# Optimization experiments

Measured on AMD Instinct MI355X. Metric: run time of the kernel, lower is better.

The kernel has to match this reference:

```python
import jax, jax.numpy as jnp
import numpy as np

NC, NG, D = 50000, 3000, 64
E_CG, E_GC, E_GG = 3_000_000, 3_000_000, 100_000
KEEP = 0.9  # 1 - drop_out


def _mask(key, n):
    return (jax.random.uniform(key, (n, 1)) < KEEP).astype(jnp.float32) / KEEP


def setup_inputs() -> dict:
    key = jax.random.key(0)
    ks = jax.random.split(key, 20)
    return {
        "c_feat": jax.random.normal(ks[0], (NC, D), jnp.float32),
        "g_feat": jax.random.normal(ks[1], (NG, D), jnp.float32),
        "cj_cell": jax.random.uniform(ks[2], (NC, 1), jnp.float32),
        "ci_cell": jax.random.uniform(ks[3], (NC, 1), jnp.float32),
        "cj_gene": jax.random.uniform(ks[4], (NG, 1), jnp.float32),
        "ci_gene": jax.random.uniform(ks[5], (NG, 1), jnp.float32),
        "cjj_gene": jax.random.uniform(ks[6], (NG, 1), jnp.float32),
        "cii_gene": jax.random.uniform(ks[7], (NG, 1), jnp.float32),
        "mask_exp": _mask(ks[8], NC),
        "mask_rev": _mask(ks[9], NG),
        "mask_gg": _mask(ks[10], NG),
        "src_cg": jax.random.randint(ks[11], (E_CG,), 0, NC, jnp.int32),
        "dst_cg": jax.random.randint(ks[12], (E_CG,), 0, NG, jnp.int32),
        "src_gc": jax.random.randint(ks[13], (E_GC,), 0, NG, jnp.int32),
        "dst_gc": jax.random.randint(ks[14], (E_GC,), 0, NC, jnp.int32),
        "src_gg": jax.random.randint(ks[15], (E_GG,), 0, NG, jnp.int32),
        "dst_gg": jax.random.randint(ks[16], (E_GG,), 0, NG, jnp.int32),
    }


def _light_conv(src_feats, cj, mask, ci, src, dst, n_dst):
    # weighted_feats = src_feats * dropout(cj); copy_u + sum; scale by ci
    wf = src_feats * (cj * mask)                      # [Nsrc, D]
    agg = jax.ops.segment_sum(wf[src], dst, num_segments=n_dst)  # [Ndst, D]
    return agg * ci


def reference(c_feat, g_feat, cj_cell, ci_cell, cj_gene, ci_gene,
              cjj_gene, cii_gene, mask_exp, mask_rev, mask_gg,
              src_cg, dst_cg, src_gc, dst_gc, src_gg, dst_gg):
    alpha1 = 0.5
    # relation 'exp': cell -> gene
    g_exp = _light_conv(c_feat, cj_cell, mask_exp, ci_gene, src_cg, dst_cg, NG)
    # relation 'reverse-exp': gene -> cell (only relation targeting cells)
    c_out = _light_conv(g_feat, cj_gene, mask_rev, ci_cell, src_gc, dst_gc, NC)
    # relation 'co-exp': gene -> gene (uses cjj/cii)
    g_gg = _light_conv(g_feat, cjj_gene, mask_gg, cii_gene, src_gg, dst_gg, NG)
    # aggregate='stack' over gene dst relations, then alpha-weighted combine
    g_out = alpha1 * g_exp + (1.0 - alpha1) * g_gg
    return (c_out, g_out)
```

## Files before the change

kernel.cpp:

```cpp
#include <hip/hip_runtime.h>

#define NC 50000
#define NG 3000
#define D  64

#define NB_CG 750
#define NB_GC 782
#define PBITS 18
#define TILE  4096
#define KTILE (TILE / 256)
#define NPREP 128
#define CAP   4608
#define KCAP  ((CAP + 255) / 256)
#define GG_CAP 128
#define OVF_CAP 262144

__device__ inline unsigned short f2bf(float x) {
    unsigned u = __float_as_uint(x);
    unsigned r = u + 0x7FFFu + ((u >> 16) & 1u);
    return (unsigned short)(r >> 16);
}

__device__ __forceinline__ void acc8(const uint4& q, float f[8]) {
    f[0] += __uint_as_float(q.x << 16); f[1] += __uint_as_float(q.x & 0xFFFF0000u);
    f[2] += __uint_as_float(q.y << 16); f[3] += __uint_as_float(q.y & 0xFFFF0000u);
    f[4] += __uint_as_float(q.z << 16); f[5] += __uint_as_float(q.z & 0xFFFF0000u);
    f[6] += __uint_as_float(q.w << 16); f[7] += __uint_as_float(q.w & 0xFFFF0000u);
}

__device__ inline void row8f(const float* feat, int s, int l8, float f[8]) {
    const float4* row = (const float4*)(feat + (size_t)s * D);
    const float4 a = row[l8];
    const float4 b = row[l8 + 8];
    f[0] = a.x; f[1] = a.y; f[2] = a.z; f[3] = a.w;
    f[4] = b.x; f[5] = b.y; f[6] = b.z; f[7] = b.w;
}


__global__ __launch_bounds__(256, 7) void partition_kernel(
    const int* __restrict__ src_cg, const int* __restrict__ dst_cg, int e_cg, int nt_cg,
    const int* __restrict__ src_gc, const int* __restrict__ dst_gc, int e_gc, int nt_gc,
    const int* __restrict__ src_gg, const int* __restrict__ dst_gg, int e_gg,
    int* __restrict__ cur_cg, int* __restrict__ cur_gc, int* __restrict__ cnt_gg,
    unsigned* __restrict__ bkt_cg, unsigned* __restrict__ bkt_gc, int* __restrict__ bkt_gg,
    int* __restrict__ ovf_cnt, uint2* __restrict__ ovf,
    const float* __restrict__ cj_cell, const float* __restrict__ mask_exp,
    const float* __restrict__ cj_gene, const float* __restrict__ mask_rev,
    const float* __restrict__ cjj_gene, const float* __restrict__ mask_gg,
    float* __restrict__ w_cell, float* __restrict__ w_rev, float* __restrict__ w_gg,
    const float* __restrict__ c_feat, const float* __restrict__ g_feat,
    unsigned short* __restrict__ wc16, unsigned short* __restrict__ wg16,
    unsigned short* __restrict__ wgg16, int do_cvt)
{
    const int tid = threadIdx.x;
    const int NT2 = nt_cg + nt_gc;

    if (blockIdx.x >= NT2 + 64) {
        const int pb = blockIdx.x - NT2 - 64;
        const long long stride = (long long)NPREP * 256;
        for (long long i = (long long)pb * 256 + tid; i < NC; i += stride)
            w_cell[i] = cj_cell[i] * mask_exp[i];
        for (long long i = (long long)pb * 256 + tid; i < NG; i += stride) {
            w_rev[i] = cj_gene[i] * mask_rev[i];
            w_gg[i]  = cjj_gene[i] * mask_gg[i];
        }
        if (do_cvt) {
            const long long total8 = (long long)(NC + NG) * D / 8;
            for (long long t = (long long)pb * 256 + tid; t < total8; t += stride) {
                const long long base = t * 8;
                if (base < (long long)NC * D) {
                    const int s = (int)(base >> 6);
                    const float w = cj_cell[s] * mask_exp[s];
                    const float4 a = ((const float4*)(c_feat + base))[0];
                    const float4 b = ((const float4*)(c_feat + base))[1];
                    unsigned short* dp = wc16 + base;
                    ((ushort4*)dp)[0] = make_ushort4(f2bf(w*a.x), f2bf(w*a.y), f2bf(w*a.z), f2bf(w*a.w));
                    ((ushort4*)dp)[1] = make_ushort4(f2bf(w*b.x), f2bf(w*b.y), f2bf(w*b.z), f2bf(w*b.w));
                } else {
                    const long long gb = base - (long long)NC * D;
                    const int s = (int)(gb >> 6);
                    const float wr = cj_gene[s] * mask_rev[s];
                    const float wg = cjj_gene[s] * mask_gg[s];
                    const float4 a = ((const float4*)(g_feat + gb))[0];
                    const float4 b = ((const float4*)(g_feat + gb))[1];
                    ((ushort4*)(wg16 + gb))[0]  = make_ushort4(f2bf(wr*a.x), f2bf(wr*a.y), f2bf(wr*a.z), f2bf(wr*a.w));
                    ((ushort4*)(wg16 + gb))[1]  = make_ushort4(f2bf(wr*b.x), f2bf(wr*b.y), f2bf(wr*b.z), f2bf(wr*b.w));
                    ((ushort4*)(wgg16 + gb))[0] = make_ushort4(f2bf(wg*a.x), f2bf(wg*a.y), f2bf(wg*a.z), f2bf(wg*a.w));
                    ((ushort4*)(wgg16 + gb))[1] = make_ushort4(f2bf(wg*b.x), f2bf(wg*b.y), f2bf(wg*b.z), f2bf(wg*b.w));
                }
            }
            if (pb == 0) {
                for (int i = tid; i < D; i += 256) {
                    wc16[(size_t)NC * D + i] = 0;
                    wg16[(size_t)NG * D + i] = 0;
                    wgg16[(size_t)NG * D + i] = 0;
                }
            }
        }
        return;
    }

    if (blockIdx.x >= NT2) {
        for (long long e = (long long)(blockIdx.x - NT2) * 256 + tid; e < e_gg;
             e += (long long)64 * 256) {
            const int dd = dst_gg[e];
            const int ss = src_gg[e];
            if ((unsigned)dd >= (unsigned)NG || (unsigned)ss >= (unsigned)NG) continue;
            const int pos = atomicAdd(&cnt_gg[dd], 1);
            if (pos < GG_CAP) bkt_gg[dd * GG_CAP + pos] = ss;
            else {
                const int op = atomicAdd(ovf_cnt, 1);
                if (op >= 0 && op < OVF_CAP)
                    ovf[op] = make_uint2((2u << 30) | (unsigned)ss, (unsigned)dd);
            }
        }
        return;
    }

    const int* src; const int* dst; int ne; int* cur; unsigned* bkt;
    int shift, nbins, t; unsigned rel;
    if (blockIdx.x < nt_cg) { src = src_cg; dst = dst_cg; ne = e_cg; cur = cur_cg; bkt = bkt_cg; shift = 2; nbins = NB_CG; t = blockIdx.x;         rel = 0u; }
    else                    { src = src_gc; dst = dst_gc; ne = e_gc; cur = cur_gc; bkt = bkt_gc; shift = 6; nbins = NB_GC; t = blockIdx.x - nt_cg; rel = 1u; }
    const long long tb = (long long)t * TILE;
    if (tb >= ne) return;
    const int n = (int)((ne - tb) < TILE ? (ne - tb) : TILE);

    __shared__ int toff[784];
    __shared__ int gsadj[784];
    __shared__ unsigned staged[TILE];
    const unsigned PMASK = (1u << PBITS) - 1u;
    const unsigned DMASK = (1u << shift) - 1u;

    for (int i = tid; i < nbins; i += 256) toff[i] = 0;

    int rd[KTILE], rs[KTILE];
    #pragma unroll
    for (int k = 0; k < KTILE; ++k) {
        const int i = k * 256 + tid;
        rd[k] = (i < n) ? dst[tb + i] : -1;
        rs[k] = (i < n) ? src[tb + i] : 0;
    }
    __syncthreads();
    #pragma unroll
    for (int k = 0; k < KTILE; ++k) {
        const unsigned b = ((unsigned)rd[k]) >> shift;
        if (b < (unsigned)nbins) atomicAdd(&toff[b], 1);
    }
    __syncthreads();
    if (tid < 64) {
        int carry = 0;
        for (int c = 0; c < nbins; c += 64) {
            int idx = c + tid;
            int v = (idx < nbins) ? toff[idx] : 0;
            int incl = v;
            #pragma unroll
            for (int d = 1; d < 64; d <<= 1) {
                int x = __shfl_up(incl, d);
                if (tid >= d) incl += x;
            }
            if (idx < nbins) {
                const int excl = incl - v + carry;
                toff[idx] = excl;
                gsadj[idx] = (v ? atomicAdd(&cur[idx], v) : 0) - excl;
            }
            carry += __shfl(incl, 63);
        }
    }
    __syncthreads();
    #pragma unroll
    for (int k = 0; k < KTILE; ++k) {
        const unsigned d = (unsigned)rd[k];
        const unsigned b = d >> shift;
        if (b < (unsigned)nbins) {
            const int p = atomicAdd(&toff[b], 1);
            if (p >= 0 && p < TILE)
                staged[p] = (b << PBITS) | ((unsigned)rs[k] << shift) | (d & DMASK);
        }
    }
    __syncthreads();
    for (int i = tid; i < n; i += 256) {
        const unsigned v = staged[i];
        const unsigned b = v >> PBITS;
        if (b < (unsigned)nbins) {
            const int local = gsadj[b] + i;
            if (local >= 0 && local < CAP) {
                bkt[(size_t)b * CAP + local] = v & PMASK;
            } else {
                const unsigned s = (v >> shift) & 0xFFFFu;
                const unsigned dd = (b << shift) | (v & DMASK);
                const int op = atomicAdd(ovf_cnt, 1);
                if (op >= 0 && op < OVF_CAP)
                    ovf[op] = make_uint2((rel << 30) | s, dd);
            }
        }
    }
}


template <bool BF16>
__global__ __launch_bounds__(256, 8) void gather3_kernel(
    const unsigned* __restrict__ bkt_cg, const int* __restrict__ cur_cg,
    const unsigned* __restrict__ bkt_gc, const int* __restrict__ cur_gc,
    const void* __restrict__ fc, const void* __restrict__ fg, const void* __restrict__ fgg,
    const float* __restrict__ craw, const float* __restrict__ graw,
    const float* __restrict__ w_cell, const float* __restrict__ w_rev, const float* __restrict__ w_gg,
    const float* __restrict__ ci_gene, const float* __restrict__ cii_gene, const float* __restrict__ ci_cell,
    const int* __restrict__ cnt_gg, const int* __restrict__ bkt_gg,
    const int* __restrict__ ovf_cnt, const uint2* __restrict__ ovf,
    float* __restrict__ g_out, float* __restrict__ c_out)
{
    __shared__ unsigned short sorted[CAP];
    __shared__ int lh[64];
    __shared__ int loff[64];

    const bool is_cg = (blockIdx.x < NB_CG);
    const int bin = is_cg ? blockIdx.x : blockIdx.x - NB_CG;
    int n = (is_cg ? cur_cg : cur_gc)[bin];
    n = n > CAP ? CAP : n;
    const long long base = (long long)bin * CAP;
    const unsigned* bkt = is_cg ? bkt_cg : bkt_gc;
    const void* feat = is_cg ? fc : fg;
    const float* wsrc = is_cg ? w_cell : w_rev;
    const int shift = is_cg ? 2 : 6;
    const int DIVv = is_cg ? 4 : 64;
    const int KPC  = is_cg ? 16 : 1;
    const int DUM  = is_cg ? NC : NG;
    const int tid  = threadIdx.x;
    const int lane = tid & 63;
    const int wid  = tid >> 6;
    const int grp8 = lane >> 3;
    const int l8   = lane & 7;

    for (int i = tid; i < 64; i += 256) lh[i] = 0;
    unsigned rv[KCAP];
    #pragma unroll
    for (int k = 0; k < KCAP; ++k) {
        const int i = k * 256 + tid;
        rv[k] = (i < n) ? bkt[base + i] : 0xFFFFFFFFu;
    }
    __syncthreads();
    #pragma unroll
    for (int k = 0; k < KCAP; ++k) {
        const unsigned v = rv[k];
        if (v != 0xFFFFFFFFu) {
            const int kk = is_cg ? (int)(((v & 3u) << 4) | (((v >> 2) & 0xFFFFu) >> 12))
                                 : (int)(v & 63u);
            atomicAdd(&lh[kk], 1);
        }
    }
    __syncthreads();
    if (tid < 64) {
        int v = lh[tid];
        int incl = v;
        #pragma unroll
        for (int d = 1; d < 64; d <<= 1) {
            int t = __shfl_up(incl, d);
            if (tid >= d) incl += t;
        }
        loff[tid] = incl - v;
        lh[tid] = 0;
    }
    __syncthreads();
    #pragma unroll
    for (int k = 0; k < KCAP; ++k) {
        const unsigned v = rv[k];
        if (v != 0xFFFFFFFFu) {
            const int kk = is_cg ? (int)(((v & 3u) << 4) | (((v >> 2) & 0xFFFFu) >> 12))
                                 : (int)(v & 63u);
            const int p = loff[kk] + atomicAdd(&lh[kk], 1);
            if (p >= 0 && p < CAP) sorted[p] = (unsigned short)((v >> shift) & 0xFFFFu);
        }
    }
    __syncthreads();

    int novf = *ovf_cnt;
    novf = novf < 0 ? 0 : (novf > OVF_CAP ? OVF_CAP : novf);

    for (int cell = wid; cell < DIVv; cell += 4) {
        const int r = (bin << shift) + cell;
        if (r >= (is_cg ? NG : NC)) continue;

        float fA[8] = {0.f, 0.f, 0.f, 0.f, 0.f, 0.f, 0.f, 0.f};
        {
            const int k0 = cell * KPC, k1 = k0 + KPC - 1;
            const int lo = loff[k0], hi = loff[k1] + lh[k1];
            if (BF16) {
                const uint4* fp = (const uint4*)feat;
                for (int jj = lo; jj < hi; jj += 32) {
                    const int b0 = jj + grp8;
                    const int s0 = (b0      < hi) ? (int)sorted[b0]      : DUM;
                    const int s1 = (b0 + 8  < hi) ? (int)sorted[b0 + 8]  : DUM;
                    const int s2 = (b0 + 16 < hi) ? (int)sorted[b0 + 16] : DUM;
                    const int s3 = (b0 + 24 < hi) ? (int)sorted[b0 + 24] : DUM;
                    const uint4 q0 = fp[(size_t)s0 * 8 + l8];
                    const uint4 q1 = fp[(size_t)s1 * 8 + l8];
                    const uint4 q2 = fp[(size_t)s2 * 8 + l8];
                    const uint4 q3 = fp[(size_t)s3 * 8 + l8];
                    acc8(q0, fA); acc8(q1, fA); acc8(q2, fA); acc8(q3, fA);
                }
            } else {
                for (int jj = lo; jj < hi; jj += 8) {
                    const int j = jj + grp8;
                    const bool valid = (j < hi);
                    const int s = valid ? (int)sorted[j] : 0;
                    const float w = valid ? wsrc[s] : 0.0f;
                    float f[8]; row8f((const float*)feat, s, l8, f);
                    #pragma unroll
                    for (int q = 0; q < 8; ++q) fA[q] += w * f[q];
                }
            }
        }

        float fB[8] = {0.f, 0.f, 0.f, 0.f, 0.f, 0.f, 0.f, 0.f};
        if (is_cg) {
            int ngg = cnt_gg[r];
            ngg = ngg > GG_CAP ? GG_CAP : ngg;
            const int* bg = bkt_gg + (size_t)r * GG_CAP;
            if (BF16) {
                const uint4* fp = (const uint4*)fgg;
                for (int jj = 0; jj < ngg; jj += 16) {
                    const int j0 = jj + grp8;
                    const int j1 = jj + 8 + grp8;
                    const int s0 = (j0 < ngg) ? bg[j0] : NG;
                    const int s1 = (j1 < ngg) ? bg[j1] : NG;
                    const uint4 q0 = fp[(size_t)s0 * 8 + l8];
                    const uint4 q1 = fp[(size_t)s1 * 8 + l8];
                    acc8(q0, fB); acc8(q1, fB);
                }
            } else {
                for (int jj = 0; jj < ngg; jj += 8) {
                    const int j = jj + grp8;
                    const bool valid = (j < ngg);
                    const int s = valid ? bg[j] : 0;
                    const float w = valid ? w_gg[s] : 0.0f;
                    float f[8]; row8f(graw, s, l8, f);
                    #pragma unroll
                    for (int q = 0; q < 8; ++q) fB[q] += w * f[q];
                }
            }
        }

        #pragma unroll
        for (int q = 0; q < 8; ++q) {
            #pragma unroll
            for (int off = 8; off < 64; off <<= 1) fA[q] += __shfl_xor(fA[q], off);
        }
        if (is_cg) {
            #pragma unroll
            for (int q = 0; q < 8; ++q) {
                #pragma unroll
                for (int off = 8; off < 64; off <<= 1) fB[q] += __shfl_xor(fB[q], off);
            }
        }

        if (grp8 == 0) {
            float o[8];
            float* outp;
            if (is_cg) {
                const float sa = 0.5f * ci_gene[r];
                const float sb = 0.5f * cii_gene[r];
                outp = g_out + (size_t)r * D;
                #pragma unroll
                for (int q = 0; q < 8; ++q) o[q] = sa * fA[q] + sb * fB[q];
            } else {
                const float sc = ci_cell[r];
                outp = c_out + (size_t)r * D;
                #pragma unroll
                for (int q = 0; q < 8; ++q) o[q] = sc * fA[q];
            }

            if (novf > 0) {
                for (int e = 0; e < novf; ++e) {
                    const uint2 vv = ovf[e];
                    const int d = (int)vv.y;
                    if (d != r) continue;
                    const unsigned relv = vv.x >> 30;
                    const int s = (int)(vv.x & 0x3FFFFFFFu);
                    const float* fr = nullptr; float w = 0.f;
                    if (is_cg) {
                        if (relv == 0u && s < NC)      { fr = craw + (size_t)s * D; w = 0.5f * ci_gene[r] * w_cell[s]; }
                        else if (relv == 2u && s < NG) { fr = graw + (size_t)s * D; w = 0.5f * cii_gene[r] * w_gg[s]; }
                    } else {
                        if (relv == 1u && s < NG)      { fr = graw + (size_t)s * D; w = ci_cell[r] * w_rev[s]; }
                    }
                    if (fr) {
                        #pragma unroll
                        for (int q = 0; q < 8; ++q) {
                            const int elem = BF16 ? (8 * l8 + q)
                                                  : (q < 4 ? 4 * l8 + q : 32 + 4 * l8 + (q - 4));
                            o[q] += w * fr[elem];
                        }
                    }
                }
            }

            if (BF16) {
                *(float4*)(outp + 8 * l8)     = make_float4(o[0], o[1], o[2], o[3]);
                *(float4*)(outp + 8 * l8 + 4) = make_float4(o[4], o[5], o[6], o[7]);
            } else {
                *(float4*)(outp + 4 * l8)      = make_float4(o[0], o[1], o[2], o[3]);
                *(float4*)(outp + 32 + 4 * l8) = make_float4(o[4], o[5], o[6], o[7]);
            }
        }
    }
}


__global__ __launch_bounds__(256) void edge_scatter_kernel(
    const float* __restrict__ feat, const float* __restrict__ cj,
    const float* __restrict__ mask, const float* __restrict__ ci,
    const int* __restrict__ src, const int* __restrict__ dst,
    float* __restrict__ out, int nedges, float alpha)
{
    const int lane16 = threadIdx.x & 15;
    const int eloc   = threadIdx.x >> 4;
    const long long e = (long long)blockIdx.x * 16 + eloc;
    if (e >= nedges) return;
    const int s = src[e];
    const int t = dst[e];
    const float w = cj[s] * mask[s] * ci[t] * alpha;
    const float4 v = *(const float4*)(feat + (size_t)s * D + lane16 * 4);
    float* o = out + (size_t)t * D + lane16 * 4;
#if defined(__HIP_DEVICE_COMPILE__)
    unsafeAtomicAdd(o + 0, w * v.x);
    unsafeAtomicAdd(o + 1, w * v.y);
    unsafeAtomicAdd(o + 2, w * v.z);
    unsafeAtomicAdd(o + 3, w * v.w);
#endif
}


extern "C" void kernel_launch(void* const* d_in, const int* in_sizes, int n_in,
                              void* d_out, int out_size, void* d_ws, size_t ws_size,
                              hipStream_t stream)
{
    const float* c_feat   = (const float*)d_in[0];
    const float* g_feat   = (const float*)d_in[1];
    const float* cj_cell  = (const float*)d_in[2];
    const float* ci_cell  = (const float*)d_in[3];
    const float* cj_gene  = (const float*)d_in[4];
    const float* ci_gene  = (const float*)d_in[5];
    const float* cjj_gene = (const float*)d_in[6];
    const float* cii_gene = (const float*)d_in[7];
    const float* mask_exp = (const float*)d_in[8];
    const float* mask_rev = (const float*)d_in[9];
    const float* mask_gg  = (const float*)d_in[10];
    const int*   src_cg   = (const int*)d_in[11];
    const int*   dst_cg   = (const int*)d_in[12];
    const int*   src_gc   = (const int*)d_in[13];
    const int*   dst_gc   = (const int*)d_in[14];
    const int*   src_gg   = (const int*)d_in[15];
    const int*   dst_gg   = (const int*)d_in[16];

    const int e_cg = in_sizes[11];
    const int e_gc = in_sizes[13];
    const int e_gg = in_sizes[15];

    float* c_out = (float*)d_out;
    float* g_out = (float*)d_out + (size_t)NC * D;

    const int nt_cg = (e_cg + TILE - 1) / TILE;
    const int nt_gc = (e_gc + TILE - 1) / TILE;

    int* ws = (int*)d_ws;
    size_t p = 0;
    int* cur_cg  = ws + p; p += NB_CG;
    int* cur_gc  = ws + p; p += NB_GC;
    int* cnt_gg  = ws + p; p += NG;
    int* ovf_cnt = ws + p; p += 1;
    const size_t zcount = p;
    float* w_cell = (float*)(ws + p); p += NC;
    float* w_rev  = (float*)(ws + p); p += NG;
    float* w_gg   = (float*)(ws + p); p += NG;
    unsigned* bkt_cg = (unsigned*)(ws + p); p += (size_t)NB_CG * CAP;
    unsigned* bkt_gc = (unsigned*)(ws + p); p += (size_t)NB_GC * CAP;
    int* bkt_gg = ws + p; p += (size_t)NG * GG_CAP;
    p = (p + 1) & ~(size_t)1;
    uint2* ovf = (uint2*)(ws + p); p += (size_t)OVF_CAP * 2;
    const size_t need_base = p * sizeof(int);
    p = (p + 3) & ~(size_t)3;
    unsigned short* wc16  = (unsigned short*)(ws + p); p += (size_t)(NC + 1) * D / 2;
    unsigned short* wg16  = (unsigned short*)(ws + p); p += (size_t)(NG + 1) * D / 2;
    unsigned short* wgg16 = (unsigned short*)(ws + p); p += (size_t)(NG + 1) * D / 2;
    const size_t need_full = p * sizeof(int);

    if (need_base > ws_size || e_cg > 3200000 || e_gc > 3200000 || e_gg > 200000) {
        hipMemsetAsync(d_out, 0, (size_t)out_size * sizeof(float), stream);
        edge_scatter_kernel<<<(e_cg + 15) / 16, 256, 0, stream>>>(
            c_feat, cj_cell, mask_exp, ci_gene, src_cg, dst_cg, g_out, e_cg, 0.5f);
        edge_scatter_kernel<<<(e_gc + 15) / 16, 256, 0, stream>>>(
            g_feat, cj_gene, mask_rev, ci_cell, src_gc, dst_gc, c_out, e_gc, 1.0f);
        edge_scatter_kernel<<<(e_gg + 15) / 16, 256, 0, stream>>>(
            g_feat, cjj_gene, mask_gg, cii_gene, src_gg, dst_gg, g_out, e_gg, 0.5f);
        return;
    }
    const int use_bf16 = (need_full <= ws_size) ? 1 : 0;

    hipMemsetAsync(ws, 0, zcount * sizeof(int), stream);

    partition_kernel<<<nt_cg + nt_gc + 64 + NPREP, 256, 0, stream>>>(
        src_cg, dst_cg, e_cg, nt_cg,
        src_gc, dst_gc, e_gc, nt_gc,
        src_gg, dst_gg, e_gg,
        cur_cg, cur_gc, cnt_gg,
        bkt_cg, bkt_gc, bkt_gg,
        ovf_cnt, ovf,
        cj_cell, mask_exp, cj_gene, mask_rev, cjj_gene, mask_gg,
        w_cell, w_rev, w_gg, c_feat, g_feat, wc16, wg16, wgg16, use_bf16);

    if (use_bf16) {
        gather3_kernel<true><<<NB_CG + NB_GC, 256, 0, stream>>>(
            bkt_cg, cur_cg, bkt_gc, cur_gc,
            (const void*)wc16, (const void*)wg16, (const void*)wgg16,
            c_feat, g_feat,
            w_cell, w_rev, w_gg, ci_gene, cii_gene, ci_cell,
            cnt_gg, bkt_gg, ovf_cnt, ovf, g_out, c_out);
    } else {
        gather3_kernel<false><<<NB_CG + NB_GC, 256, 0, stream>>>(
            bkt_cg, cur_cg, bkt_gc, cur_gc,
            (const void*)c_feat, (const void*)g_feat, (const void*)g_feat,
            c_feat, g_feat,
            w_cell, w_rev, w_gg, ci_gene, cii_gene, ci_cell,
            cnt_gg, bkt_gg, ovf_cnt, ovf, g_out, c_out);
    }
}
```

Baseline: 244.0 us.

## Split each gather bin across two blocks, using atomic accumulation for gene outputs

Launches twice as many gather blocks, each handling half of a bin. Cell-to-gene bins split their source subkeys between halves, and the two partial sums are combined into g_out with atomic adds after a memset. Gene-to-cell bins split their destination rows. This raises parallelism and occupancy for the gather phase. The cost is that each block reloads the full bucket, and it adds a g_out memset and float atomics.

```diff
diff --git a/kernel.cpp b/kernel.cpp
--- a/kernel.cpp
+++ b/kernel.cpp
@@ -213,8 +213,10 @@
     __shared__ int lh[64];
     __shared__ int loff[64];
 
-    const bool is_cg = (blockIdx.x < NB_CG);
-    const int bin = is_cg ? blockIdx.x : blockIdx.x - NB_CG;
+    const int bid = blockIdx.x;
+    const bool is_cg = (bid < 2 * NB_CG);
+    const int bin  = is_cg ? (bid >> 1) : ((bid - 2 * NB_CG) >> 1);
+    const int half = is_cg ? (bid & 1)  : ((bid - 2 * NB_CG) & 1);
     int n = (is_cg ? cur_cg : cur_gc)[bin];
     n = n > CAP ? CAP : n;
     const long long base = (long long)bin * CAP;
@@ -222,8 +224,6 @@
     const void* feat = is_cg ? fc : fg;
     const float* wsrc = is_cg ? w_cell : w_rev;
     const int shift = is_cg ? 2 : 6;
-    const int DIVv = is_cg ? 4 : 64;
-    const int KPC  = is_cg ? 16 : 1;
     const int DUM  = is_cg ? NC : NG;
     const int tid  = threadIdx.x;
     const int lane = tid & 63;
@@ -245,7 +245,8 @@
         if (v != 0xFFFFFFFFu) {
             const int kk = is_cg ? (int)(((v & 3u) << 4) | (((v >> 2) & 0xFFFFu) >> 12))
                                  : (int)(v & 63u);
-            atomicAdd(&lh[kk], 1);
+            const bool mine = is_cg ? (((kk >> 3) & 1) == half) : ((kk >> 5) == half);
+            if (mine) atomicAdd(&lh[kk], 1);
         }
     }
     __syncthreads();
@@ -267,8 +268,11 @@
         if (v != 0xFFFFFFFFu) {
             const int kk = is_cg ? (int)(((v & 3u) << 4) | (((v >> 2) & 0xFFFFu) >> 12))
                                  : (int)(v & 63u);
-            const int p = loff[kk] + atomicAdd(&lh[kk], 1);
-            if (p >= 0 && p < CAP) sorted[p] = (unsigned short)((v >> shift) & 0xFFFFu);
+            const bool mine = is_cg ? (((kk >> 3) & 1) == half) : ((kk >> 5) == half);
+            if (mine) {
+                const int p = loff[kk] + atomicAdd(&lh[kk], 1);
+                if (p >= 0 && p < CAP) sorted[p] = (unsigned short)((v >> shift) & 0xFFFFu);
+            }
         }
     }
     __syncthreads();
@@ -276,13 +280,17 @@
     int novf = *ovf_cnt;
     novf = novf < 0 ? 0 : (novf > OVF_CAP ? OVF_CAP : novf);
 
-    for (int cell = wid; cell < DIVv; cell += 4) {
+    const int cellLo = is_cg ? 0 : half * 32;
+    const int cellHi = is_cg ? 4 : half * 32 + 32;
+
+    for (int cell = cellLo + wid; cell < cellHi; cell += 4) {
         const int r = (bin << shift) + cell;
         if (r >= (is_cg ? NG : NC)) continue;
 
         float fA[8] = {0.f, 0.f, 0.f, 0.f, 0.f, 0.f, 0.f, 0.f};
         {
-            const int k0 = cell * KPC, k1 = k0 + KPC - 1;
+            const int k0 = is_cg ? (cell * 16 + 8 * half) : cell;
+            const int k1 = is_cg ? (k0 + 7) : cell;
             const int lo = loff[k0], hi = loff[k1] + lh[k1];
             if (BF16) {
                 const uint4* fp = (const uint4*)feat;
@@ -312,7 +320,7 @@
         }
 
         float fB[8] = {0.f, 0.f, 0.f, 0.f, 0.f, 0.f, 0.f, 0.f};
-        if (is_cg) {
+        if (is_cg && half == 0) {
             int ngg = cnt_gg[r];
             ngg = ngg > GG_CAP ? GG_CAP : ngg;
             const int* bg = bkt_gg + (size_t)r * GG_CAP;
@@ -345,7 +353,7 @@
             #pragma unroll
             for (int off = 8; off < 64; off <<= 1) fA[q] += __shfl_xor(fA[q], off);
         }
-        if (is_cg) {
+        if (is_cg && half == 0) {
             #pragma unroll
             for (int q = 0; q < 8; ++q) {
                 #pragma unroll
@@ -355,51 +363,71 @@
 
         if (grp8 == 0) {
             float o[8];
-            float* outp;
             if (is_cg) {
                 const float sa = 0.5f * ci_gene[r];
                 const float sb = 0.5f * cii_gene[r];
-                outp = g_out + (size_t)r * D;
                 #pragma unroll
                 for (int q = 0; q < 8; ++q) o[q] = sa * fA[q] + sb * fB[q];
+                float* outp = g_out + (size_t)r * D;
+
+                if (half == 0 && novf > 0) {
+                    for (int e = 0; e < novf; ++e) {
+                        const uint2 vv = ovf[e];
+                        if ((int)vv.y != r) continue;
+                        const unsigned relv = vv.x >> 30;
+                        const int s = (int)(vv.x & 0x3FFFFFFFu);
+                        const float* fr = nullptr; float w = 0.f;
+                        if (relv == 0u && s < NC)      { fr = craw + (size_t)s * D; w = 0.5f * ci_gene[r] * w_cell[s]; }
+                        else if (relv == 2u && s < NG) { fr = graw + (size_t)s * D; w = 0.5f * cii_gene[r] * w_gg[s]; }
+                        if (fr) {
+                            #pragma unroll
+                            for (int q = 0; q < 8; ++q) {
+                                const int elem = BF16 ? (8 * l8 + q)
+                                                      : (q < 4 ? 4 * l8 + q : 32 + 4 * l8 + (q - 4));
+                                o[q] += w * fr[elem];
+                            }
+                        }
+                    }
+                }
+#if defined(__HIP_DEVICE_COMPILE__)
+                #pragma unroll
+                for (int q = 0; q < 8; ++q) {
+                    const int elem = BF16 ? (8 * l8 + q)
+                                          : (q < 4 ? 4 * l8 + q : 32 + 4 * l8 + (q - 4));
+                    unsafeAtomicAdd(outp + elem, o[q]);
+                }
+#endif
             } else {
                 const float sc = ci_cell[r];
-                outp = c_out + (size_t)r * D;
+                float* outp = c_out + (size_t)r * D;
                 #pragma unroll
                 for (int q = 0; q < 8; ++q) o[q] = sc * fA[q];
-            }
-
-            if (novf > 0) {
-                for (int e = 0; e < novf; ++e) {
-                    const uint2 vv = ovf[e];
-                    const int d = (int)vv.y;
-                    if (d != r) continue;
-                    const unsigned relv = vv.x >> 30;
-                    const int s = (int)(vv.x & 0x3FFFFFFFu);
-                    const float* fr = nullptr; float w = 0.f;
-                    if (is_cg) {
-                        if (relv == 0u && s < NC)      { fr = craw + (size_t)s * D; w = 0.5f * ci_gene[r] * w_cell[s]; }
-                        else if (relv == 2u && s < NG) { fr = graw + (size_t)s * D; w = 0.5f * cii_gene[r] * w_gg[s]; }
-                    } else {
-                        if (relv == 1u && s < NG)      { fr = graw + (size_t)s * D; w = ci_cell[r] * w_rev[s]; }
-                    }
-                    if (fr) {
-                        #pragma unroll
-                        for (int q = 0; q < 8; ++q) {
-                            const int elem = BF16 ? (8 * l8 + q)
-                                                  : (q < 4 ? 4 * l8 + q : 32 + 4 * l8 + (q - 4));
-                            o[q] += w * fr[elem];
+
+                if (novf > 0) {
+                    for (int e = 0; e < novf; ++e) {
+                        const uint2 vv = ovf[e];
+                        if ((int)vv.y != r) continue;
+                        const unsigned relv = vv.x >> 30;
+                        const int s = (int)(vv.x & 0x3FFFFFFFu);
+                        if (relv == 1u && s < NG) {
+                            const float* fr = graw + (size_t)s * D;
+                            const float w = ci_cell[r] * w_rev[s];
+                            #pragma unroll
+                            for (int q = 0; q < 8; ++q) {
+                                const int elem = BF16 ? (8 * l8 + q)
+                                                      : (q < 4 ? 4 * l8 + q : 32 + 4 * l8 + (q - 4));
+                                o[q] += w * fr[elem];
+                            }
                         }
                     }
                 }
-            }
-
-            if (BF16) {
-                *(float4*)(outp + 8 * l8)     = make_float4(o[0], o[1], o[2], o[3]);
-                *(float4*)(outp + 8 * l8 + 4) = make_float4(o[4], o[5], o[6], o[7]);
-            } else {
-                *(float4*)(outp + 4 * l8)      = make_float4(o[0], o[1], o[2], o[3]);
-                *(float4*)(outp + 32 + 4 * l8) = make_float4(o[4], o[5], o[6], o[7]);
+                if (BF16) {
+                    *(float4*)(outp + 8 * l8)     = make_float4(o[0], o[1], o[2], o[3]);
+                    *(float4*)(outp + 8 * l8 + 4) = make_float4(o[4], o[5], o[6], o[7]);
+                } else {
+                    *(float4*)(outp + 4 * l8)      = make_float4(o[0], o[1], o[2], o[3]);
+                    *(float4*)(outp + 32 + 4 * l8) = make_float4(o[4], o[5], o[6], o[7]);
+                }
             }
         }
     }
@@ -497,6 +525,7 @@
     const int use_bf16 = (need_full <= ws_size) ? 1 : 0;
 
     hipMemsetAsync(ws, 0, zcount * sizeof(int), stream);
+    hipMemsetAsync(g_out, 0, (size_t)NG * D * sizeof(float), stream);
 
     partition_kernel<<<nt_cg + nt_gc + 64 + NPREP, 256, 0, stream>>>(
         src_cg, dst_cg, e_cg, nt_cg,
@@ -508,15 +537,16 @@
         cj_cell, mask_exp, cj_gene, mask_rev, cjj_gene, mask_gg,
         w_cell, w_rev, w_gg, c_feat, g_feat, wc16, wg16, wgg16, use_bf16);
 
+    const int ngather = 2 * (NB_CG + NB_GC);
     if (use_bf16) {
-        gather3_kernel<true><<<NB_CG + NB_GC, 256, 0, stream>>>(
+        gather3_kernel<true><<<ngather, 256, 0, stream>>>(
             bkt_cg, cur_cg, bkt_gc, cur_gc,
             (const void*)wc16, (const void*)wg16, (const void*)wgg16,
             c_feat, g_feat,
             w_cell, w_rev, w_gg, ci_gene, cii_gene, ci_cell,
             cnt_gg, bkt_gg, ovf_cnt, ovf, g_out, c_out);
     } else {
-        gather3_kernel<false><<<NB_CG + NB_GC, 256, 0, stream>>>(
+        gather3_kernel<false><<<ngather, 256, 0, stream>>>(
             bkt_cg, cur_cg, bkt_gc, cur_gc,
             (const void*)c_feat, (const void*)g_feat, (const void*)g_feat,
             c_feat, g_feat,
```

New measurement: 253.5 us. 3.9% more time.

## Split gather3 feature dimension across two block halves and reduce cg rows in shared memory

Applied to the files above, without the earlier changes.

Launches twice as many gather blocks, each handling 32 of the 64 feature columns, so each source row load is half as wide and more blocks are in flight. In the BF16 path each 8-lane group now issues eight narrower loads per iteration into two accumulators. For cell-to-gene bins, all four warps' partial sums go to shared memory, and only warp 0 gathers gene-gene edges. The first 32 threads then finish the four gene rows serially, with per-column scalar gathers for the gene-gene edges of rows 1-3. This duplicates the bucket sort and histogram work in both halves, and the serial tail plus per-thread scalar loads may offset the gain. The layout of the cg branch looks fragile: it breaks out of the row loop after the first row and carries leftover no-op code.

```diff
diff --git a/kernel.cpp b/kernel.cpp
--- a/kernel.cpp
+++ b/kernel.cpp
@@ -21,19 +21,9 @@
     return (unsigned short)(r >> 16);
 }
 
-__device__ __forceinline__ void acc8(const uint4& q, float f[8]) {
+__device__ __forceinline__ void acc4(const uint2& q, float f[4]) {
     f[0] += __uint_as_float(q.x << 16); f[1] += __uint_as_float(q.x & 0xFFFF0000u);
     f[2] += __uint_as_float(q.y << 16); f[3] += __uint_as_float(q.y & 0xFFFF0000u);
-    f[4] += __uint_as_float(q.z << 16); f[5] += __uint_as_float(q.z & 0xFFFF0000u);
-    f[6] += __uint_as_float(q.w << 16); f[7] += __uint_as_float(q.w & 0xFFFF0000u);
-}
-
-__device__ inline void row8f(const float* feat, int s, int l8, float f[8]) {
-    const float4* row = (const float4*)(feat + (size_t)s * D);
-    const float4 a = row[l8];
-    const float4 b = row[l8 + 8];
-    f[0] = a.x; f[1] = a.y; f[2] = a.z; f[3] = a.w;
-    f[4] = b.x; f[5] = b.y; f[6] = b.z; f[7] = b.w;
 }
 
 
@@ -212,9 +202,13 @@
     __shared__ unsigned short sorted[CAP];
     __shared__ int lh[64];
     __shared__ int loff[64];
-
-    const bool is_cg = (blockIdx.x < NB_CG);
-    const int bin = is_cg ? blockIdx.x : blockIdx.x - NB_CG;
+    __shared__ float part[5][32];
+
+    const int nb1 = NB_CG + NB_GC;
+    const int half = (blockIdx.x >= nb1) ? 1 : 0;
+    const int b2 = blockIdx.x - half * nb1;
+    const bool is_cg = (b2 < NB_CG);
+    const int bin = is_cg ? b2 : b2 - NB_CG;
     int n = (is_cg ? cur_cg : cur_gc)[bin];
     n = n > CAP ? CAP : n;
     const long long base = (long long)bin * CAP;
@@ -230,6 +224,8 @@
     const int wid  = tid >> 6;
     const int grp8 = lane >> 3;
     const int l8   = lane & 7;
+    const int dimoff = 32 * half;
+    const int qoff = 8 * half + l8;
 
     for (int i = tid; i < 64; i += 256) lh[i] = 0;
     unsigned rv[KCAP];
@@ -280,52 +276,66 @@
         const int r = (bin << shift) + cell;
         if (r >= (is_cg ? NG : NC)) continue;
 
-        float fA[8] = {0.f, 0.f, 0.f, 0.f, 0.f, 0.f, 0.f, 0.f};
+        float fA[4]  = {0.f, 0.f, 0.f, 0.f};
+        float fA2[4] = {0.f, 0.f, 0.f, 0.f};
         {
             const int k0 = cell * KPC, k1 = k0 + KPC - 1;
             const int lo = loff[k0], hi = loff[k1] + lh[k1];
             if (BF16) {
-                const uint4* fp = (const uint4*)feat;
-                for (int jj = lo; jj < hi; jj += 32) {
+                const uint2* fp = (const uint2*)feat;
+                for (int jj = lo; jj < hi; jj += 64) {
                     const int b0 = jj + grp8;
                     const int s0 = (b0      < hi) ? (int)sorted[b0]      : DUM;
                     const int s1 = (b0 + 8  < hi) ? (int)sorted[b0 + 8]  : DUM;
                     const int s2 = (b0 + 16 < hi) ? (int)sorted[b0 + 16] : DUM;
                     const int s3 = (b0 + 24 < hi) ? (int)sorted[b0 + 24] : DUM;
-                    const uint4 q0 = fp[(size_t)s0 * 8 + l8];
-                    const uint4 q1 = fp[(size_t)s1 * 8 + l8];
-                    const uint4 q2 = fp[(size_t)s2 * 8 + l8];
-                    const uint4 q3 = fp[(size_t)s3 * 8 + l8];
-                    acc8(q0, fA); acc8(q1, fA); acc8(q2, fA); acc8(q3, fA);
+                    const int s4 = (b0 + 32 < hi) ? (int)sorted[b0 + 32] : DUM;
+                    const int s5 = (b0 + 40 < hi) ? (int)sorted[b0 + 40] : DUM;
+                    const int s6 = (b0 + 48 < hi) ? (int)sorted[b0 + 48] : DUM;
+                    const int s7 = (b0 + 56 < hi) ? (int)sorted[b0 + 56] : DUM;
+                    const uint2 q0 = fp[(size_t)s0 * 16 + qoff];
+                    const uint2 q1 = fp[(size_t)s1 * 16 + qoff];
+                    const uint2 q2 = fp[(size_t)s2 * 16 + qoff];
+                    const uint2 q3 = fp[(size_t)s3 * 16 + qoff];
+                    const uint2 q4 = fp[(size_t)s4 * 16 + qoff];
+                    const uint2 q5 = fp[(size_t)s5 * 16 + qoff];
+                    const uint2 q6 = fp[(size_t)s6 * 16 + qoff];
+                    const uint2 q7 = fp[(size_t)s7 * 16 + qoff];
+                    acc4(q0, fA);  acc4(q1, fA2);
+                    acc4(q2, fA);  acc4(q3, fA2);
+                    acc4(q4, fA);  acc4(q5, fA2);
+                    acc4(q6, fA);  acc4(q7, fA2);
                 }
             } else {
+                const float* ff = (const float*)feat;
                 for (int jj = lo; jj < hi; jj += 8) {
                     const int j = jj + grp8;
                     const bool valid = (j < hi);
                     const int s = valid ? (int)sorted[j] : 0;
                     const float w = valid ? wsrc[s] : 0.0f;
-                    float f[8]; row8f((const float*)feat, s, l8, f);
-                    #pragma unroll
-                    for (int q = 0; q < 8; ++q) fA[q] += w * f[q];
-                }
-            }
-        }
-
-        float fB[8] = {0.f, 0.f, 0.f, 0.f, 0.f, 0.f, 0.f, 0.f};
-        if (is_cg) {
+                    const float4 f = *(const float4*)(ff + (size_t)s * D + dimoff + 4 * l8);
+                    fA[0] += w * f.x; fA[1] += w * f.y; fA[2] += w * f.z; fA[3] += w * f.w;
+                }
+            }
+        }
+        #pragma unroll
+        for (int q = 0; q < 4; ++q) fA[q] += fA2[q];
+
+        float fB[4] = {0.f, 0.f, 0.f, 0.f};
+        if (is_cg && wid == 0) {
             int ngg = cnt_gg[r];
             ngg = ngg > GG_CAP ? GG_CAP : ngg;
             const int* bg = bkt_gg + (size_t)r * GG_CAP;
             if (BF16) {
-                const uint4* fp = (const uint4*)fgg;
+                const uint2* fp = (const uint2*)fgg;
                 for (int jj = 0; jj < ngg; jj += 16) {
                     const int j0 = jj + grp8;
                     const int j1 = jj + 8 + grp8;
                     const int s0 = (j0 < ngg) ? bg[j0] : NG;
                     const int s1 = (j1 < ngg) ? bg[j1] : NG;
-                    const uint4 q0 = fp[(size_t)s0 * 8 + l8];
-                    const uint4 q1 = fp[(size_t)s1 * 8 + l8];
-                    acc8(q0, fB); acc8(q1, fB);
+                    const uint2 q0 = fp[(size_t)s0 * 16 + qoff];
+                    const uint2 q1 = fp[(size_t)s1 * 16 + qoff];
+                    acc4(q0, fB); acc4(q1, fB);
                 }
             } else {
                 for (int jj = 0; jj < ngg; jj += 8) {
@@ -333,73 +343,108 @@
                     const bool valid = (j < ngg);
                     const int s = valid ? bg[j] : 0;
                     const float w = valid ? w_gg[s] : 0.0f;
-                    float f[8]; row8f(graw, s, l8, f);
-                    #pragma unroll
-                    for (int q = 0; q < 8; ++q) fB[q] += w * f[q];
+                    const float4 f = *(const float4*)(graw + (size_t)s * D + dimoff + 4 * l8);
+                    fB[0] += w * f.x; fB[1] += w * f.y; fB[2] += w * f.z; fB[3] += w * f.w;
                 }
             }
         }
 
         #pragma unroll
-        for (int q = 0; q < 8; ++q) {
+        for (int q = 0; q < 4; ++q) {
             #pragma unroll
             for (int off = 8; off < 64; off <<= 1) fA[q] += __shfl_xor(fA[q], off);
         }
-        if (is_cg) {
+        if (is_cg && wid == 0) {
             #pragma unroll
-            for (int q = 0; q < 8; ++q) {
+            for (int q = 0; q < 4; ++q) {
                 #pragma unroll
                 for (int off = 8; off < 64; off <<= 1) fB[q] += __shfl_xor(fB[q], off);
             }
         }
 
-        if (grp8 == 0) {
-            float o[8];
-            float* outp;
-            if (is_cg) {
-                const float sa = 0.5f * ci_gene[r];
-                const float sb = 0.5f * cii_gene[r];
-                outp = g_out + (size_t)r * D;
+        if (is_cg) {
+            if (grp8 == 0) {
                 #pragma unroll
-                for (int q = 0; q < 8; ++q) o[q] = sa * fA[q] + sb * fB[q];
-            } else {
-                const float sc = ci_cell[r];
-                outp = c_out + (size_t)r * D;
+                for (int q = 0; q < 4; ++q) part[wid][4 * l8 + q] = fA[q];
+                if (wid == 0) {
+                    #pragma unroll
+                    for (int q = 0; q < 4; ++q) part[4][4 * l8 + q] = fB[q];
+                }
+            }
+            __syncthreads();
+            if (tid < 32) {
+                const int g = (bin << 2) + 0;
+                (void)g;
+            }
+            __syncthreads();
+            if (tid < 32) {
                 #pragma unroll
-                for (int q = 0; q < 8; ++q) o[q] = sc * fA[q];
-            }
-
-            if (novf > 0) {
-                for (int e = 0; e < novf; ++e) {
-                    const uint2 vv = ovf[e];
-                    const int d = (int)vv.y;
-                    if (d != r) continue;
-                    const unsigned relv = vv.x >> 30;
-                    const int s = (int)(vv.x & 0x3FFFFFFFu);
-                    const float* fr = nullptr; float w = 0.f;
-                    if (is_cg) {
-                        if (relv == 0u && s < NC)      { fr = craw + (size_t)s * D; w = 0.5f * ci_gene[r] * w_cell[s]; }
-                        else if (relv == 2u && s < NG) { fr = graw + (size_t)s * D; w = 0.5f * cii_gene[r] * w_gg[s]; }
-                    } else {
-                        if (relv == 1u && s < NG)      { fr = graw + (size_t)s * D; w = ci_cell[r] * w_rev[s]; }
+                for (int w = 0; w < 4; ++w) {
+                    const int g = (bin << 2) + w;
+                    float o = 0.5f * ci_gene[g] * part[w][tid];
+                    if (w == 0) o += 0.5f * cii_gene[g] * part[4][tid];
+                    else {
                     }
-                    if (fr) {
-                        #pragma unroll
-                        for (int q = 0; q < 8; ++q) {
-                            const int elem = BF16 ? (8 * l8 + q)
-                                                  : (q < 4 ? 4 * l8 + q : 32 + 4 * l8 + (q - 4));
-                            o[q] += w * fr[elem];
+                    if (w != 0) {
+                        int ngg = cnt_gg[g];
+                        ngg = ngg > GG_CAP ? GG_CAP : ngg;
+                        const int* bg = bkt_gg + (size_t)g * GG_CAP;
+                        if (BF16) {
+                            const unsigned short* wp = (const unsigned short*)fgg;
+                            float acc = 0.f;
+                            for (int j = 0; j < ngg; ++j) {
+                                const int s = bg[j];
+                                const unsigned short h = wp[(size_t)s * D + dimoff + tid];
+                                acc += __uint_as_float(((unsigned)h) << 16);
+                            }
+                            o += 0.5f * cii_gene[g] * acc;
+                        } else {
+                            float acc = 0.f;
+                            for (int j = 0; j < ngg; ++j) {
+                                const int s = bg[j];
+                                acc += w_gg[s] * graw[(size_t)s * D + dimoff + tid];
+                            }
+                            o += 0.5f * cii_gene[g] * acc;
                         }
                     }
-                }
-            }
-
-            if (BF16) {
-                *(float4*)(outp + 8 * l8)     = make_float4(o[0], o[1], o[2], o[3]);
-                *(float4*)(outp + 8 * l8 + 4) = make_float4(o[4], o[5], o[6], o[7]);
-            } else {
-                *(float4*)(outp + 4 * l8)      = make_float4(o[0], o[1], o[2], o[3]);
-                *(float4*)(outp + 32 + 4 * l8) = make_float4(o[4], o[5], o[6], o[7]);
+                    if (novf > 0) {
+                        for (int e = 0; e < novf; ++e) {
+                            const uint2 vv = ovf[e];
+                            if ((int)vv.y != g) continue;
+                            const unsigned relv = vv.x >> 30;
+                            const int s = (int)(vv.x & 0x3FFFFFFFu);
+                            if (relv == 0u && s < NC)
+                                o += 0.5f * ci_gene[g] * w_cell[s] * craw[(size_t)s * D + dimoff + tid];
+                            else if (relv == 2u && s < NG)
+                                o += 0.5f * cii_gene[g] * w_gg[s] * graw[(size_t)s * D + dimoff + tid];
+                        }
+                    }
+                    g_out[(size_t)g * D + dimoff + tid] = o;
+                }
+            }
+            break;
+        } else {
+            if (grp8 == 0) {
+                const float sc = ci_cell[r];
+                float o[4];
+                #pragma unroll
+                for (int q = 0; q < 4; ++q) o[q] = sc * fA[q];
+                if (novf > 0) {
+                    for (int e = 0; e < novf; ++e) {
+                        const uint2 vv = ovf[e];
+                        if ((int)vv.y != r) continue;
+                        const unsigned relv = vv.x >> 30;
+                        const int s = (int)(vv.x & 0x3FFFFFFFu);
+                        if (relv == 1u && s < NG) {
+                            const float w = sc * w_rev[s];
+                            #pragma unroll
+                            for (int q = 0; q < 4; ++q)
+                                o[q] += w * graw[(size_t)s * D + dimoff + 4 * l8 + q];
+                        }
+                    }
+                }
+                *(float4*)(c_out + (size_t)r * D + dimoff + 4 * l8) =
+                    make_float4(o[0], o[1], o[2], o[3]);
             }
         }
     }
@@ -508,15 +553,16 @@
         cj_cell, mask_exp, cj_gene, mask_rev, cjj_gene, mask_gg,
         w_cell, w_rev, w_gg, c_feat, g_feat, wc16, wg16, wgg16, use_bf16);
 
+    const int ngather = 2 * (NB_CG + NB_GC);
     if (use_bf16) {
-        gather3_kernel<true><<<NB_CG + NB_GC, 256, 0, stream>>>(
+        gather3_kernel<true><<<ngather, 256, 0, stream>>>(
             bkt_cg, cur_cg, bkt_gc, cur_gc,
             (const void*)wc16, (const void*)wg16, (const void*)wgg16,
             c_feat, g_feat,
             w_cell, w_rev, w_gg, ci_gene, cii_gene, ci_cell,
             cnt_gg, bkt_gg, ovf_cnt, ovf, g_out, c_out);
     } else {
-        gather3_kernel<false><<<NB_CG + NB_GC, 256, 0, stream>>>(
+        gather3_kernel<false><<<ngather, 256, 0, stream>>>(
             bkt_cg, cur_cg, bkt_gc, cur_gc,
             (const void*)c_feat, (const void*)g_feat, (const void*)g_feat,
             c_feat, g_feat,
```

New measurement: 294.4 us. +20.7%, slower.
